# Kernel optimization log

Measured on AMD Instinct MI355X. Metric: run time of the kernel, lower is better.

The kernel has to match this reference:

```python
import jax, jax.numpy as jnp
import numpy as np

B, T, I, H, O, D = 64, 256, 256, 512, 256, 16


def setup_inputs() -> dict:
    key = jax.random.key(0)
    ks = jax.random.split(key, 7)
    bound_a = 1.0 / np.sqrt(I)
    bound_e = 1.0 / np.sqrt(H)
    xav = np.sqrt(6.0 / (H + H))  # xavier_uniform bound for lateral
    return {
        "x": jax.random.normal(ks[0], (B, T, I), dtype=jnp.float32),
        "w_afferent": jax.random.uniform(ks[1], (H, I), minval=-bound_a, maxval=bound_a, dtype=jnp.float32),
        "b_afferent": jax.random.uniform(ks[2], (H,), minval=-bound_a, maxval=bound_a, dtype=jnp.float32),
        "lateral": jax.random.uniform(ks[3], (H, H), minval=-xav, maxval=xav, dtype=jnp.float32),
        "tau": D * jax.random.uniform(ks[4], (H, H), dtype=jnp.float32) + 1.0,
        "w_efferent": jax.random.uniform(ks[5], (O, H), minval=-bound_e, maxval=bound_e, dtype=jnp.float32),
        "b_efferent": jax.random.uniform(ks[6], (O,), minval=-bound_e, maxval=bound_e, dtype=jnp.float32),
        "max_delay": D,
    }


def _forward(x, w_afferent, b_afferent, lateral, tau, w_efferent, b_efferent, max_delay):
    sigma = max_delay / 2.0
    inv_sigma = 1.0 / sigma
    batch, time, _ = x.shape
    hidden = lateral.shape[0]
    nslots = max_delay + 1

    # credit matrix: [nslots, H_out, H_in]
    tau_c = jnp.clip(tau, 1.0, float(max_delay))[None, :, :]
    d = jnp.arange(nslots, dtype=x.dtype)[:, None, None]
    credit = jax.nn.relu(-jnp.abs((d - tau_c) * inv_sigma**2) + inv_sigma)
    cm = credit * lateral[None, :, :]  # [nslots, h, i]

    slot_ids = jnp.arange(nslots)

    def step(carry, x_t):
        buf, ptr = carry  # buf: [nslots, B, H]
        h_delayed = buf[ptr]  # [B, H] (dynamic gather)
        h = jnp.tanh(x_t @ w_afferent.T + b_afferent + h_delayed)  # [B, H]
        scattered = jnp.einsum('dhi,bi->dbh', cm, h)  # [nslots, B, H]
        buf = buf + jnp.roll(scattered, ptr, axis=0)
        buf = buf * (slot_ids != ptr)[:, None, None].astype(buf.dtype)
        y_t = h_delayed @ w_efferent.T + b_efferent  # [B, O]
        return (buf, (ptr + 1) % nslots), y_t

    buf0 = jnp.zeros((nslots, batch, hidden), dtype=x.dtype)
    (_, _), ys = jax.lax.scan(step, (buf0, jnp.int32(0)), jnp.swapaxes(x, 0, 1))
    return ys[-1]  # [B, O], matches torch forward returning y[:, -1, :]


def reference(x, w_afferent, b_afferent, lateral, tau, w_efferent, b_efferent, max_delay):
    return _forward(x, w_afferent, b_afferent, lateral, tau, w_efferent, b_efferent, max_delay)
```

## Files before the change

kernel.cpp:

```cpp
#include <hip/hip_runtime.h>
#include <hip/hip_bf16.h>

typedef unsigned short u16;
typedef unsigned int u32;
typedef __bf16 bf16x8 __attribute__((ext_vector_type(8)));
typedef _Float16 f16x8 __attribute__((ext_vector_type(8)));
typedef float f32x4 __attribute__((ext_vector_type(4)));

#define B_ 64
#define T_ 256
#define I_ 256
#define H_ 512
#define O_ 256
#define D_ 16
#define NWG 128
#define CM_SCALE 64.0f
#define CM_INV   0.015625f

__device__ __forceinline__ bf16x8 ld_bf8(const u16* p){
  uint4 u = *(const uint4*)p;
  return __builtin_bit_cast(bf16x8, u);
}

__global__ __launch_bounds__(256) void k_split(const float* __restrict__ src,
    u16* __restrict__ hi, u16* __restrict__ lo, int n){
  int i = blockIdx.x*256 + threadIdx.x;
  if (i >= n) return;
  float v = src[i];
  __bf16 h = (__bf16)v;
  __bf16 l = (__bf16)(v - (float)h);
  hi[i] = __builtin_bit_cast(u16, h);
  lo[i] = __builtin_bit_cast(u16, l);
}

__global__ __launch_bounds__(256) void k_prep_cm(const float* __restrict__ tau,
    const float* __restrict__ lat, _Float16* __restrict__ cmf){
  int idx = blockIdx.x*256 + threadIdx.x;
  if (idx >= D_*H_*H_) return;
  int d = idx / (H_*H_) + 1;
  int r = idx % (H_*H_);
  float tc = fminf(fmaxf(tau[r], 1.0f), (float)D_);
  float cr = fmaxf(0.0f, 0.125f - fabsf((float)d - tc) * 0.015625f);
  cmf[idx] = (_Float16)(cr * lat[r] * CM_SCALE);
}

__global__ __launch_bounds__(256) void k_aff(const u16* __restrict__ xhi,
    const u16* __restrict__ xlo, const u16* __restrict__ wahi,
    const u16* __restrict__ walo, const float* __restrict__ ba,
    float* __restrict__ acc, float* __restrict__ aff_last){
  int g = blockIdx.x;
  int mg = g >> 2, ng = g & 3;
  int tid = threadIdx.x;
  int w = tid >> 6, l = tid & 63;
  int lr = l & 15, lk8 = (l >> 4) * 8;
  f32x4 accr[4][2];
  #pragma unroll
  for (int a=0;a<4;++a){ accr[a][0]=(f32x4){0.f,0.f,0.f,0.f}; accr[a][1]=(f32x4){0.f,0.f,0.f,0.f}; }
  #pragma unroll 1
  for (int kk = 0; kk < 8; ++kk){
    int i = kk*32 + lk8;
    bf16x8 ahi[4], alo[4];
    #pragma unroll
    for (int mt = 0; mt < 4; ++mt){
      int r = mg*64 + mt*16 + lr;
      int t = r >> 6, b = r & 63;
      size_t off = ((size_t)b*T_ + t)*I_ + i;
      ahi[mt] = ld_bf8(xhi + off);
      alo[mt] = ld_bf8(xlo + off);
    }
    #pragma unroll
    for (int nj = 0; nj < 2; ++nj){
      int ho = ng*128 + w*32 + nj*16 + lr;
      bf16x8 bhi = ld_bf8(wahi + (size_t)ho*I_ + i);
      bf16x8 blo = ld_bf8(walo + (size_t)ho*I_ + i);
      #pragma unroll
      for (int mt = 0; mt < 4; ++mt){
        accr[mt][nj] = __builtin_amdgcn_mfma_f32_16x16x32_bf16(ahi[mt], bhi, accr[mt][nj],0,0,0);
        accr[mt][nj] = __builtin_amdgcn_mfma_f32_16x16x32_bf16(alo[mt], bhi, accr[mt][nj],0,0,0);
        accr[mt][nj] = __builtin_amdgcn_mfma_f32_16x16x32_bf16(ahi[mt], blo, accr[mt][nj],0,0,0);
      }
    }
  }
  #pragma unroll
  for (int mt=0; mt<4; ++mt)
    #pragma unroll
    for (int nj=0; nj<2; ++nj){
      int ho = ng*128 + w*32 + nj*16 + lr;
      float bias = ba[ho];
      #pragma unroll
      for (int r2=0;r2<4;++r2){
        int r = mg*64 + mt*16 + (l>>4)*4 + r2;
        float v = accr[mt][nj][r2] + bias;
        acc[(size_t)r*H_ + ho] = v;
        if ((r >> 6) == T_-1) aff_last[(size_t)(r & 63)*H_ + ho] = v;
      }
    }
}

__global__ __launch_bounds__(256) void k_rec(const _Float16* __restrict__ cmf,
    float* __restrict__ acc, int* __restrict__ ctr){
  __shared__ char lds[98304];
  char* ldsB = lds;
  char* ldsA = lds + 65536;
  const int g = blockIdx.x;
  const int n = g & 3;
  const int k = g >> 2;
  const int d = (k >> 1) + 1;
  const int i0 = (k & 1) * 256;
  const int tid = threadIdx.x;
  const int w = tid >> 6, l = tid & 63;
  const int lr = l & 15, lkg = l >> 4;

  for (int it = tid; it < 4096; it += 256){
    int ho = it >> 5;
    int c8 = (it & 31) * 8;
    f16x8 v = *(const f16x8*)(cmf + (((size_t)(d-1)*H_ + n*128 + ho)*H_ + i0 + c8));
    int byte = (ho*512 + c8*2) ^ ((ho & 7) << 4);
    *(f16x8*)(ldsB + byte) = v;
  }
  __syncthreads();

  const int arow = tid >> 2;
  const int q    = tid & 3;
  const int cofs = q + ((arow & 1) << 2);

  for (int t = 0; t < T_; ++t){
    if (t >= d){
      if (tid == 0){
        while (__hip_atomic_load(ctr + (t-d), __ATOMIC_RELAXED, __HIP_MEMORY_SCOPE_AGENT) < NWG)
          __builtin_amdgcn_s_sleep(1);
      }
      __syncthreads();

      {
        f32x4 arr[16];
        const float* srow = acc + ((size_t)(t-d)*B_ + arow)*H_ + i0;
        #pragma unroll
        for (int j = 0; j < 8; ++j){
          int c = (4*j + cofs) & 31;
          asm volatile("global_load_dwordx4 %0, %1, off sc0 sc1"
                       : "=v"(arr[2*j])   : "v"(srow + c*8));
          asm volatile("global_load_dwordx4 %0, %1, off sc0 sc1"
                       : "=v"(arr[2*j+1]) : "v"(srow + c*8 + 4));
        }
        asm volatile("s_waitcnt vmcnt(0)" ::: "memory");
        __builtin_amdgcn_sched_barrier(0);
        #pragma unroll
        for (int j = 0; j < 8; ++j){
          int c = (4*j + cofs) & 31;
          f16x8 hh;
          #pragma unroll
          for (int e = 0; e < 8; ++e){
            float x = arr[2*j + (e>>2)][e & 3];
            float ex = __expf(2.0f * x);
            float hv = 1.0f - __fdividef(2.0f, ex + 1.0f);
            hh[e] = (_Float16)hv;
          }
          int byte = (arow*512 + c*16) ^ ((arow & 7) << 4);
          *(f16x8*)(ldsA + byte) = hh;
        }
      }
      __syncthreads();

      f32x4 accr[4][2];
      #pragma unroll
      for (int a=0;a<4;++a){ accr[a][0]=(f32x4){0.f,0.f,0.f,0.f}; accr[a][1]=(f32x4){0.f,0.f,0.f,0.f}; }
      #pragma unroll 1
      for (int kk = 0; kk < 8; ++kk){
        int kb = (kk*32 + lkg*8) * 2;
        f16x8 afr[4];
        #pragma unroll
        for (int mt = 0; mt < 4; ++mt){
          int row = mt*16 + lr;
          afr[mt] = *(const f16x8*)(ldsA + ((row*512 + kb) ^ ((row & 7) << 4)));
        }
        #pragma unroll
        for (int nj = 0; nj < 2; ++nj){
          int ho = w*32 + nj*16 + lr;
          f16x8 bfr = *(const f16x8*)(ldsB + ((ho*512 + kb) ^ ((ho & 7) << 4)));
          #pragma unroll
          for (int mt = 0; mt < 4; ++mt)
            accr[mt][nj] = __builtin_amdgcn_mfma_f32_16x16x32_f16(afr[mt], bfr, accr[mt][nj],0,0,0);
        }
      }

      float* dst = acc + (size_t)t*B_*H_ + n*128;
      #pragma unroll
      for (int mt=0; mt<4; ++mt)
        #pragma unroll
        for (int nj=0; nj<2; ++nj){
          int ho = w*32 + nj*16 + lr;
          #pragma unroll
          for (int r2=0;r2<4;++r2){
            int b = mt*16 + (l>>4)*4 + r2;
            atomicAdd(dst + (size_t)b*H_ + ho, accr[mt][nj][r2] * CM_INV);
          }
        }
    }

    asm volatile("s_waitcnt vmcnt(0)" ::: "memory");
    __syncthreads();
    if (tid == 0)
      __hip_atomic_fetch_add(ctr + t, 1, __ATOMIC_RELAXED, __HIP_MEMORY_SCOPE_AGENT);
  }
}

__global__ __launch_bounds__(256) void k_out(const float* __restrict__ acc255,
    const float* __restrict__ aff_last, const float* __restrict__ we,
    const float* __restrict__ be, float* __restrict__ y){
  int idx = blockIdx.x*256 + threadIdx.x;
  int b = idx >> 8, o = idx & 255;
  const float4* pa = (const float4*)(acc255 + (size_t)b*H_);
  const float4* pf = (const float4*)(aff_last + (size_t)b*H_);
  const float4* wb = (const float4*)(we + (size_t)o*H_);
  float s = 0.f;
  #pragma unroll 8
  for (int i2 = 0; i2 < H_/4; ++i2){
    float4 p = pa[i2], f = pf[i2], q = wb[i2];
    s += (p.x-f.x)*q.x + (p.y-f.y)*q.y + (p.z-f.z)*q.z + (p.w-f.w)*q.w;
  }
  y[idx] = s + be[o];
}

extern "C" void kernel_launch(void* const* d_in, const int* in_sizes, int n_in,
                              void* d_out, int out_size, void* d_ws, size_t ws_size,
                              hipStream_t stream){
  (void)in_sizes; (void)n_in; (void)out_size; (void)ws_size;
  const float* x   = (const float*)d_in[0];
  const float* wa  = (const float*)d_in[1];
  const float* ba  = (const float*)d_in[2];
  const float* lat = (const float*)d_in[3];
  const float* tau = (const float*)d_in[4];
  const float* we  = (const float*)d_in[5];
  const float* be  = (const float*)d_in[6];
  float* y = (float*)d_out;

  char* ws = (char*)d_ws;
  size_t cur = 0;
  auto alloc = [&](size_t sz) -> void* {
    void* p = ws + cur;
    cur += (sz + 255) & ~(size_t)255;
    return p;
  };
  int*      ctr      = (int*)     alloc(4096);
  float*    acc      = (float*)   alloc((size_t)T_*B_*H_*4);
  float*    aff_last = (float*)   alloc((size_t)B_*H_*4);
  u16*      xhi      = (u16*)     alloc((size_t)B_*T_*I_*2);
  u16*      xlo      = (u16*)     alloc((size_t)B_*T_*I_*2);
  u16*      wahi     = (u16*)     alloc((size_t)H_*I_*2);
  u16*      walo     = (u16*)     alloc((size_t)H_*I_*2);
  _Float16* cmf      = (_Float16*)alloc((size_t)D_*H_*H_*2);

  hipMemsetAsync(ctr, 0, 4096, stream);

  k_split<<<(B_*T_*I_+255)/256, 256, 0, stream>>>(x, xhi, xlo, B_*T_*I_);
  k_split<<<(H_*I_+255)/256,   256, 0, stream>>>(wa, wahi, walo, H_*I_);
  k_prep_cm<<<(D_*H_*H_+255)/256, 256, 0, stream>>>(tau, lat, cmf);
  k_aff<<<1024, 256, 0, stream>>>(xhi, xlo, wahi, walo, ba, acc, aff_last);
  k_rec<<<NWG, 256, 0, stream>>>(cmf, acc, ctr);
  k_out<<<(B_*O_+255)/256, 256, 0, stream>>>(acc + (size_t)(T_-1)*B_*H_, aff_last, we, be, y);
}
```

Before: 2.737 ms.

## Merge two delay slots per workgroup to halve recurrent workgroup count

```diff
diff --git a/kernel.cpp b/kernel.cpp
--- a/kernel.cpp
+++ b/kernel.cpp
@@ -13,7 +13,7 @@
 #define H_ 512
 #define O_ 256
 #define D_ 16
-#define NWG 128
+#define NWG 64
 #define CM_SCALE 64.0f
 #define CM_INV   0.015625f
 
@@ -97,16 +97,20 @@
     }
 }
 
-__global__ __launch_bounds__(256) void k_rec(const _Float16* __restrict__ cmf,
+__global__ __launch_bounds__(256,1) void k_rec(const _Float16* __restrict__ cmf,
     float* __restrict__ acc, int* __restrict__ ctr){
-  __shared__ char lds[98304];
-  char* ldsB = lds;
-  char* ldsA = lds + 65536;
+  __shared__ char lds[131072];
+  char* ldsB0 = lds;
+  char* ldsA0 = lds + 65536;
+  char* ldsA1 = lds + 98304;
   const int g = blockIdx.x;
   const int n = g & 3;
-  const int k = g >> 2;
-  const int d = (k >> 1) + 1;
-  const int i0 = (k & 1) * 256;
+  const int p = g >> 2;
+  const int half = p & 1;
+  const int jp = p >> 1;
+  const int d0 = 2*jp + 1;
+  const int d1 = 2*jp + 2;
+  const int i0 = half * 256;
   const int tid = threadIdx.x;
   const int w = tid >> 6, l = tid & 63;
   const int lr = l & 15, lkg = l >> 4;
@@ -114,9 +118,17 @@
   for (int it = tid; it < 4096; it += 256){
     int ho = it >> 5;
     int c8 = (it & 31) * 8;
-    f16x8 v = *(const f16x8*)(cmf + (((size_t)(d-1)*H_ + n*128 + ho)*H_ + i0 + c8));
+    f16x8 v = *(const f16x8*)(cmf + (((size_t)(d0-1)*H_ + n*128 + ho)*H_ + i0 + c8));
     int byte = (ho*512 + c8*2) ^ ((ho & 7) << 4);
-    *(f16x8*)(ldsB + byte) = v;
+    *(f16x8*)(ldsB0 + byte) = v;
+  }
+  f16x8 bfr1[2][8];
+  #pragma unroll
+  for (int nj = 0; nj < 2; ++nj){
+    const _Float16* bp = cmf + (((size_t)(d1-1)*H_ + n*128 + w*32 + nj*16 + lr)*H_ + i0);
+    #pragma unroll
+    for (int kk = 0; kk < 8; ++kk)
+      bfr1[nj][kk] = *(const f16x8*)(bp + kk*32 + lkg*8);
   }
   __syncthreads();
 
@@ -125,23 +137,35 @@
   const int cofs = q + ((arow & 1) << 2);
 
   for (int t = 0; t < T_; ++t){
-    if (t >= d){
+    if (t >= d0){
       if (tid == 0){
-        while (__hip_atomic_load(ctr + (t-d), __ATOMIC_RELAXED, __HIP_MEMORY_SCOPE_AGENT) < NWG)
+        while (__hip_atomic_load(ctr + (t-d0), __ATOMIC_RELAXED, __HIP_MEMORY_SCOPE_AGENT) < NWG)
           __builtin_amdgcn_s_sleep(1);
       }
       __syncthreads();
 
+      const bool do1 = (t >= d1);
       {
-        f32x4 arr[16];
-        const float* srow = acc + ((size_t)(t-d)*B_ + arow)*H_ + i0;
+        f32x4 a0[16], a1[16];
+        const float* s0 = acc + ((size_t)(t-d0)*B_ + arow)*H_ + i0;
         #pragma unroll
         for (int j = 0; j < 8; ++j){
           int c = (4*j + cofs) & 31;
           asm volatile("global_load_dwordx4 %0, %1, off sc0 sc1"
-                       : "=v"(arr[2*j])   : "v"(srow + c*8));
+                       : "=v"(a0[2*j])   : "v"(s0 + c*8));
           asm volatile("global_load_dwordx4 %0, %1, off sc0 sc1"
-                       : "=v"(arr[2*j+1]) : "v"(srow + c*8 + 4));
+                       : "=v"(a0[2*j+1]) : "v"(s0 + c*8 + 4));
+        }
+        if (do1){
+          const float* s1 = acc + ((size_t)(t-d1)*B_ + arow)*H_ + i0;
+          #pragma unroll
+          for (int j = 0; j < 8; ++j){
+            int c = (4*j + cofs) & 31;
+            asm volatile("global_load_dwordx4 %0, %1, off sc0 sc1"
+                         : "=v"(a1[2*j])   : "v"(s1 + c*8));
+            asm volatile("global_load_dwordx4 %0, %1, off sc0 sc1"
+                         : "=v"(a1[2*j+1]) : "v"(s1 + c*8 + 4));
+          }
         }
         asm volatile("s_waitcnt vmcnt(0)" ::: "memory");
         __builtin_amdgcn_sched_barrier(0);
@@ -151,13 +175,29 @@
           f16x8 hh;
           #pragma unroll
           for (int e = 0; e < 8; ++e){
-            float x = arr[2*j + (e>>2)][e & 3];
+            float x = a0[2*j + (e>>2)][e & 3];
             float ex = __expf(2.0f * x);
             float hv = 1.0f - __fdividef(2.0f, ex + 1.0f);
             hh[e] = (_Float16)hv;
           }
           int byte = (arow*512 + c*16) ^ ((arow & 7) << 4);
-          *(f16x8*)(ldsA + byte) = hh;
+          *(f16x8*)(ldsA0 + byte) = hh;
+        }
+        if (do1){
+          #pragma unroll
+          for (int j = 0; j < 8; ++j){
+            int c = (4*j + cofs) & 31;
+            f16x8 hh;
+            #pragma unroll
+            for (int e = 0; e < 8; ++e){
+              float x = a1[2*j + (e>>2)][e & 3];
+              float ex = __expf(2.0f * x);
+              float hv = 1.0f - __fdividef(2.0f, ex + 1.0f);
+              hh[e] = (_Float16)hv;
+            }
+            int byte = (arow*512 + c*16) ^ ((arow & 7) << 4);
+            *(f16x8*)(ldsA1 + byte) = hh;
+          }
         }
       }
       __syncthreads();
@@ -172,15 +212,32 @@
         #pragma unroll
         for (int mt = 0; mt < 4; ++mt){
           int row = mt*16 + lr;
-          afr[mt] = *(const f16x8*)(ldsA + ((row*512 + kb) ^ ((row & 7) << 4)));
+          afr[mt] = *(const f16x8*)(ldsA0 + ((row*512 + kb) ^ ((row & 7) << 4)));
         }
         #pragma unroll
         for (int nj = 0; nj < 2; ++nj){
           int ho = w*32 + nj*16 + lr;
-          f16x8 bfr = *(const f16x8*)(ldsB + ((ho*512 + kb) ^ ((ho & 7) << 4)));
+          f16x8 bfr = *(const f16x8*)(ldsB0 + ((ho*512 + kb) ^ ((ho & 7) << 4)));
           #pragma unroll
           for (int mt = 0; mt < 4; ++mt)
             accr[mt][nj] = __builtin_amdgcn_mfma_f32_16x16x32_f16(afr[mt], bfr, accr[mt][nj],0,0,0);
+        }
+      }
+      if (do1){
+        #pragma unroll 1
+        for (int kk = 0; kk < 8; ++kk){
+          int kb = (kk*32 + lkg*8) * 2;
+          f16x8 afr[4];
+          #pragma unroll
+          for (int mt = 0; mt < 4; ++mt){
+            int row = mt*16 + lr;
+            afr[mt] = *(const f16x8*)(ldsA1 + ((row*512 + kb) ^ ((row & 7) << 4)));
+          }
+          #pragma unroll
+          for (int nj = 0; nj < 2; ++nj)
+            #pragma unroll
+            for (int mt = 0; mt < 4; ++mt)
+              accr[mt][nj] = __builtin_amdgcn_mfma_f32_16x16x32_f16(afr[mt], bfr1[nj][kk], accr[mt][nj],0,0,0);
         }
       }
 
```

Measured after the change: 3.274 ms. +19.6%, slower.
